# Performance work log

Hardware: AMD Instinct MI355X
Metric: run time of the kernel (lower is better)

Reference implementation:

```python
import jax, jax.numpy as jnp
import numpy as np

B, C, H, W = 8, 64, 64, 64
CI = 32  # inter_channels = in_channels // 2
EPS = 1e-5


def conv1x1(x, w, b=None):
    # x: (b,c,h,w), w: (o,c) -> (b,o,h,w)
    y = jnp.einsum('bchw,oc->bohw', x, w)
    if b is not None:
        y = y + b[None, :, None, None]
    return y


def maxpool2x2(x):
    b, c, h, w = x.shape
    return x.reshape(b, c, h // 2, 2, w // 2, 2).max(axis=(3, 5))


def setup_inputs() -> dict:
    key = jax.random.key(0)
    ks = jax.random.split(key, 12)
    s = 0.05
    return {
        'x': jax.random.normal(ks[0], (B, C, H, W), jnp.float32),
        'theta_w': jax.random.normal(ks[1], (CI, C), jnp.float32) * s,
        'theta_b': jax.random.normal(ks[2], (CI,), jnp.float32) * s,
        'phi_w': jax.random.normal(ks[3], (CI, C), jnp.float32) * s,
        'phi_b': jax.random.normal(ks[4], (CI,), jnp.float32) * s,
        'psi_w': jax.random.normal(ks[5], (CI, C), jnp.float32) * s,
        'psi_b': jax.random.normal(ks[6], (CI,), jnp.float32) * s,
        'cp_w': jax.random.normal(ks[7], (2 * CI,), jnp.float32) * s,  # concat_project 1x1, no bias
        'W_w': jax.random.normal(ks[8], (C, CI + 1), jnp.float32) * s,
        'W_b': jax.random.normal(ks[9], (C,), jnp.float32) * s,
        'bn_gamma': jax.random.normal(ks[10], (C,), jnp.float32) * s + 1.0,
        'bn_beta': jax.random.normal(ks[11], (C,), jnp.float32) * s,
    }


def reference(x, theta_w, theta_b, phi_w, phi_b, psi_w, psi_b, cp_w, W_w, W_b, bn_gamma, bn_beta):
    b = x.shape[0]
    # psi / phi branches get 2x2 maxpool (sub_sample=True default)
    psi_x = maxpool2x2(conv1x1(x, psi_w, psi_b)).reshape(b, CI, -1)      # (b,ci,M)
    psi_x = psi_x.transpose(0, 2, 1)                                     # (b,M,ci)
    theta_x = conv1x1(x, theta_w, theta_b).reshape(b, CI, -1)            # (b,ci,N)
    phi_x = maxpool2x2(conv1x1(x, phi_w, phi_b)).reshape(b, CI, -1)      # (b,ci,M)
    # concat_project(cat[theta_i, phi_j]) + ReLU == relu(w1.theta_i + w2.phi_j)
    w1, w2 = cp_w[:CI], cp_w[CI:]
    a = jnp.einsum('bcn,c->bn', theta_x, w1)                             # (b,N)
    bb = jnp.einsum('bcm,c->bm', phi_x, w2)                              # (b,M)
    f = jax.nn.relu(a[:, :, None] + bb[:, None, :])                      # (b,N,M)
    M = f.shape[-1]
    f_div_C = f / float(M)
    y = jnp.matmul(f_div_C, psi_x)                                       # (b,N,ci)
    y = y.transpose(0, 2, 1).reshape(b, CI, H, W)
    # r_structure_type='zero' -> zero structure channel
    structure_feat = jnp.zeros((b, 1, H, W), y.dtype)
    y = jnp.concatenate([y, structure_feat], axis=1)                     # (b,ci+1,H,W)
    wy = conv1x1(y, W_w, W_b)                                            # (b,C,H,W)
    # BatchNorm2d, training-mode batch stats, biased variance
    mu = wy.mean(axis=(0, 2, 3), keepdims=True)
    var = wy.var(axis=(0, 2, 3), keepdims=True)
    wy = (wy - mu) * jax.lax.rsqrt(var + EPS)
    wy = wy * bn_gamma[None, :, None, None] + bn_beta[None, :, None, None]
    return wy + x
```

## Files before the change

kernel.cpp:

```cpp
#include <hip/hip_runtime.h>

#define OFF_A    0
#define OFF_BB   32768
#define OFF_SBB  40960
#define OFF_PERM 49152
#define OFF_U    57344
#define OFF_T1   581632
#define OFF_T2   1106432
#define OFF_KK   1631232
#define OFF_M    1664000

__global__ __launch_bounds__(256) void kA(
    const float* __restrict__ x, const float* __restrict__ theta_w,
    const float* __restrict__ theta_b, const float* __restrict__ phi_w,
    const float* __restrict__ phi_b, const float* __restrict__ psi_w,
    const float* __restrict__ psi_b, const float* __restrict__ cp_w,
    const float* __restrict__ Ww, float* ws)
{
    __shared__ float sm[4160];
    __shared__ float spsi[8*33];
    __shared__ float sWw[64*33];
    int tid = threadIdx.x;
    int bid = blockIdx.x;
    if (bid < 1024) {
        for (int e = tid; e < 2048; e += 256) {
            int i = e >> 6, c = e & 63;
            sm[i*65 + c]        = phi_w[e];
            sm[2080 + i*65 + c] = psi_w[e];
        }
        for (int e = tid; e < 2048; e += 256)
            sWw[(e >> 5)*33 + (e & 31)] = Ww[(e >> 5)*33 + (e & 31)];
        __syncthreads();
        int t = (bid << 8) + tid;
        int i = t & 31;
        int m = (t >> 5) & 1023;
        int b = t >> 15;
        int ph = m >> 5, pw = m & 31;
        const float* xb = x + b*262144 + ph*128 + pw*2;
        const float* rp = sm + i*65;
        const float* rs = sm + 2080 + i*65;
        float p0=0,p1=0,p2=0,p3=0,s0=0,s1=0,s2=0,s3=0;
        #pragma unroll 8
        for (int c = 0; c < 64; ++c) {
            float2 xa = *(const float2*)(xb + c*4096);
            float2 xc = *(const float2*)(xb + c*4096 + 64);
            float wp = rp[c], wv = rs[c];
            p0 += xa.x*wp; p1 += xa.y*wp; p2 += xc.x*wp; p3 += xc.y*wp;
            s0 += xa.x*wv; s1 += xa.y*wv; s2 += xc.x*wv; s3 += xc.y*wv;
        }
        float pv = fmaxf(fmaxf(p0,p1), fmaxf(p2,p3)) + phi_b[i];
        float sv = fmaxf(fmaxf(s0,s1), fmaxf(s2,s3)) + psi_b[i];
        spsi[(tid >> 5)*33 + i] = sv;
        float v = pv * cp_w[32 + i];
        v += __shfl_xor(v, 16, 32);
        v += __shfl_xor(v,  8, 32);
        v += __shfl_xor(v,  4, 32);
        v += __shfl_xor(v,  2, 32);
        v += __shfl_xor(v,  1, 32);
        if (i == 0) ws[OFF_BB + (b<<10) + m] = v;
        __syncthreads();
        int m0 = (bid & 127) << 3;
        #pragma unroll
        for (int rep = 0; rep < 2; ++rep) {
            int idx = tid + (rep << 8);
            int ml = idx >> 6, o = idx & 63;
            const float* pr = &spsi[ml*33];
            const float* wr = &sWw[o*33];
            float u = 0;
            #pragma unroll
            for (int i2 = 0; i2 < 32; ++i2) u += pr[i2]*wr[i2];
            ws[OFF_U + (((b<<10) + m0 + ml) << 6) + o] = u;
        }
    } else {
        if (bid == 1024 && tid < 128) ws[OFF_M + tid] = 0.0f;
        if (tid < 64) {
            float s = 0;
            for (int i = 0; i < 32; ++i) s += cp_w[i]*theta_w[i*64 + tid];
            sm[tid] = s;
        } else if (tid == 64) {
            float s = 0;
            for (int i = 0; i < 32; ++i) s += cp_w[i]*theta_b[i];
            sm[64] = s;
        }
        __syncthreads();
        int t = ((bid - 1024) << 8) + tid;
        int n = t & 4095, b = t >> 12;
        const float* xb = x + b*262144 + n;
        float acc = sm[64];
        #pragma unroll 8
        for (int c = 0; c < 64; ++c) acc += xb[c*4096]*sm[c];
        ws[OFF_A + t] = acc;
    }
}

__global__ __launch_bounds__(256) void kRank(float* ws)
{
    __shared__ float sb[1024];
    int tid = threadIdx.x;
    int b = blockIdx.x >> 5, chunk = blockIdx.x & 31;
    const float* bb = ws + OFF_BB + (b<<10);
    for (int e = tid; e < 1024; e += 256) sb[e] = bb[e];
    __syncthreads();
    int ml = tid >> 3, jl = tid & 7;
    int m = (chunk<<5) + ml;
    float v = sb[m];
    int cnt = 0;
    for (int s = 0; s < 128; ++s) {
        int j = jl + (s<<3);
        float u = sb[j];
        cnt += (u > v || (u == v && j < m)) ? 1 : 0;
    }
    cnt += __shfl_xor(cnt, 1, 8);
    cnt += __shfl_xor(cnt, 2, 8);
    cnt += __shfl_xor(cnt, 4, 8);
    if (jl == 0) {
        ws[OFF_SBB + (b<<10) + cnt] = v;
        ((int*)ws)[OFF_PERM + (b<<10) + cnt] = m;
    }
}

__global__ __launch_bounds__(1024) void kPS(float* ws)
{
    __shared__ float ssort[1024];
    __shared__ int   sperm[1024];
    __shared__ float sc1[1024];
    __shared__ float sc2[1024];
    __shared__ float hcnt[1025], hsa[1025], hsa2[1025];
    int tid = threadIdx.x;
    int b = blockIdx.x >> 1, oh = blockIdx.x & 1;
    int obase = oh << 5;
    ssort[tid] = ws[OFF_SBB + (b<<10) + tid];
    sperm[tid] = ((const int*)ws)[OFF_PERM + (b<<10) + tid];
    for (int e = tid; e < 1025; e += 1024) { hcnt[e]=0; hsa[e]=0; hsa2[e]=0; }
    __syncthreads();
    const float* ag = ws + OFF_A + (b<<12);
    int* kk = (int*)ws + OFF_KK + (b<<12);
    for (int q = 0; q < 4; ++q) {
        int n = (q<<10) + tid;
        float av = ag[n];
        float tt = -av;
        int lo = 0, hi = 1024;
        #pragma unroll
        for (int s = 0; s < 10; ++s) {
            int mid = (lo+hi)>>1;
            if (ssort[mid] > tt) lo = mid+1; else hi = mid;
        }
        if (oh == 0) kk[n] = lo;
        atomicAdd(&hcnt[lo], 1.0f);
        atomicAdd(&hsa[lo], av);
        atomicAdd(&hsa2[lo], av*av);
    }
    __syncthreads();
    int o = tid & 31, ch = tid >> 5;
    const float* Ub = ws + OFF_U + (b<<16);
    float s1 = 0, s2 = 0;
    for (int jl = 0; jl < 32; ++jl) {
        int jj = (ch<<5) + jl;
        float p = Ub[(sperm[jj]<<6) + obase + o];
        s1 += p; s2 += ssort[jj]*p;
    }
    sc1[(ch<<5)+o] = s1; sc2[(ch<<5)+o] = s2;
    __syncthreads();
    if (tid < 32) {
        float run = 0;
        for (int c = 0; c < 32; ++c) { float t = sc1[(c<<5)+tid]; sc1[(c<<5)+tid] = run; run += t; }
    } else if (tid < 64) {
        int o2 = tid - 32;
        float run = 0;
        for (int c = 0; c < 32; ++c) { float t = sc2[(c<<5)+o2]; sc2[(c<<5)+o2] = run; run += t; }
    }
    __syncthreads();
    float run1 = sc1[(ch<<5)+o], run2 = sc2[(ch<<5)+o];
    float* T1 = ws + OFF_T1 + b*65600;
    float* T2 = ws + OFF_T2 + b*65600;
    if (tid < 32) { T1[obase + tid] = 0.0f; T2[obase + tid] = 0.0f; }
    const float inv = 1.0f/1024.0f;
    float m1 = 0, m2 = 0;
    for (int jl = 0; jl < 32; ++jl) {
        int jj = (ch<<5) + jl;
        float p = Ub[(sperm[jj]<<6) + obase + o];
        run1 += p; run2 += ssort[jj]*p;
        float t1 = run1*inv, t2 = run2*inv;
        int k = jj + 1;
        T1[(k<<6) + obase + o] = t1;
        T2[(k<<6) + obase + o] = t2;
        float c = hcnt[k], sa = hsa[k], sa2 = hsa2[k];
        m1 += sa*t1 + c*t2;
        m2 += sa2*t1*t1 + 2.0f*sa*t1*t2 + c*t2*t2;
    }
    __syncthreads();
    sc1[(ch<<5)+o] = m1; sc2[(ch<<5)+o] = m2;
    __syncthreads();
    if (tid < 32) {
        float s = 0;
        for (int c = 0; c < 32; ++c) s += sc1[(c<<5)+tid];
        atomicAdd(&ws[OFF_M + obase + tid], s);
    } else if (tid < 64) {
        int o2 = tid - 32;
        float s = 0;
        for (int c = 0; c < 32; ++c) s += sc2[(c<<5)+o2];
        atomicAdd(&ws[OFF_M + 64 + obase + o2], s);
    }
}

__global__ __launch_bounds__(256) void kFinal(
    const float* __restrict__ x, const float* __restrict__ Wb,
    const float* __restrict__ gamma, const float* __restrict__ beta,
    const float* __restrict__ ws, float* __restrict__ out)
{
    __shared__ float tile[64*65];
    __shared__ float sa[64];
    __shared__ int   sk[64];
    __shared__ float sA[64];
    __shared__ float sD[64];
    int tid = threadIdx.x;
    int b = blockIdx.x >> 6;
    int n0 = (blockIdx.x & 63) << 6;
    if (tid < 64) {
        sa[tid] = ws[OFF_A + (b<<12) + n0 + tid];
        sk[tid] = ((const int*)ws)[OFF_KK + (b<<12) + n0 + tid];
        const float Ninv = 1.0f/32768.0f;
        float m1 = ws[OFF_M + tid] * Ninv;
        float m2 = ws[OFF_M + 64 + tid] * Ninv;
        float wb = Wb[tid];
        float mu  = m1 + wb;
        float E2  = m2 + 2.0f*wb*m1 + wb*wb;
        float var = E2 - mu*mu;
        float A = gamma[tid] * rsqrtf(var + 1e-5f);
        sA[tid] = A;
        sD[tid] = beta[tid] + A*(wb - mu);
    }
    __syncthreads();
    const float* T1 = ws + OFF_T1 + b*65600;
    const float* T2 = ws + OFF_T2 + b*65600;
    {
        int o = tid & 63, ng = tid >> 6;
        float Ao = sA[o], Do = sD[o];
        for (int j = 0; j < 16; ++j) {
            int n = (ng << 4) + j;
            int k = sk[n];
            float a = sa[n];
            float t1 = T1[(k<<6) + o];
            float t2 = T2[(k<<6) + o];
            tile[o*65 + n] = Ao*(a*t1 + t2) + Do;
        }
    }
    __syncthreads();
    {
        int n = tid & 63, og = tid >> 6;
        for (int j = 0; j < 16; ++j) {
            int o = (og << 4) + j;
            int idx = ((b<<6) + o)*4096 + n0 + n;
            out[idx] = tile[o*65 + n] + x[idx];
        }
    }
}

extern "C" void kernel_launch(void* const* d_in, const int* in_sizes, int n_in,
                              void* d_out, int out_size, void* d_ws, size_t ws_size,
                              hipStream_t stream)
{
    const float* x       = (const float*)d_in[0];
    const float* theta_w = (const float*)d_in[1];
    const float* theta_b = (const float*)d_in[2];
    const float* phi_w   = (const float*)d_in[3];
    const float* phi_b   = (const float*)d_in[4];
    const float* psi_w   = (const float*)d_in[5];
    const float* psi_b   = (const float*)d_in[6];
    const float* cp_w    = (const float*)d_in[7];
    const float* Ww      = (const float*)d_in[8];
    const float* Wb      = (const float*)d_in[9];
    const float* gamma   = (const float*)d_in[10];
    const float* beta    = (const float*)d_in[11];
    float* ws  = (float*)d_ws;
    float* out = (float*)d_out;

    kA<<<1152, 256, 0, stream>>>(x, theta_w, theta_b, phi_w, phi_b,
                                 psi_w, psi_b, cp_w, Ww, ws);
    kRank<<<256, 256, 0, stream>>>(ws);
    kPS<<<16, 1024, 0, stream>>>(ws);
    kFinal<<<512, 256, 0, stream>>>(x, Wb, gamma, beta, ws, out);
}
```

Before: 143.0 us.

## Move threshold histogram into rank kernel and widen prefix-scan kernel across blocks

Computes the per-query insertion index and histograms by brute-force counting in kRank, accumulating them with global atomics, so kPS no longer does a binary search and shared histogram. kPS now runs 64 blocks of 8 output channels each instead of 16 blocks of 32. Its prefix scan uses wave shuffles plus a small cross-wave pass rather than serial shared-memory scans. Psi values are held in registers so U is read once. This raises parallelism in the serial-bottleneck kernel, at the cost of extra global atomics and a larger zero-init in kA.

```diff
diff --git a/kernel.cpp b/kernel.cpp
--- a/kernel.cpp
+++ b/kernel.cpp
@@ -9,6 +9,9 @@
 #define OFF_T2   1106432
 #define OFF_KK   1631232
 #define OFF_M    1664000
+#define OFF_HC   1664128
+#define OFF_HS   1672328
+#define OFF_HS2  1680528
 
 __global__ __launch_bounds__(256) void kA(
     const float* __restrict__ x, const float* __restrict__ theta_w,
@@ -72,7 +75,9 @@
             ws[OFF_U + (((b<<10) + m0 + ml) << 6) + o] = u;
         }
     } else {
-        if (bid == 1024 && tid < 128) ws[OFF_M + tid] = 0.0f;
+        if (bid == 1024) {
+            for (int e = tid; e < 24728; e += 256) ws[OFF_M + e] = 0.0f;
+        }
         if (tid < 64) {
             float s = 0;
             for (int i = 0; i < 32; ++i) s += cp_w[i]*theta_w[i*64 + tid];
@@ -101,21 +106,43 @@
     const float* bb = ws + OFF_BB + (b<<10);
     for (int e = tid; e < 1024; e += 256) sb[e] = bb[e];
     __syncthreads();
-    int ml = tid >> 3, jl = tid & 7;
-    int m = (chunk<<5) + ml;
-    float v = sb[m];
-    int cnt = 0;
-    for (int s = 0; s < 128; ++s) {
-        int j = jl + (s<<3);
-        float u = sb[j];
-        cnt += (u > v || (u == v && j < m)) ? 1 : 0;
-    }
-    cnt += __shfl_xor(cnt, 1, 8);
-    cnt += __shfl_xor(cnt, 2, 8);
-    cnt += __shfl_xor(cnt, 4, 8);
-    if (jl == 0) {
-        ws[OFF_SBB + (b<<10) + cnt] = v;
-        ((int*)ws)[OFF_PERM + (b<<10) + cnt] = m;
+    {
+        int ml = tid >> 3, jl = tid & 7;
+        int m = (chunk<<5) + ml;
+        float v = sb[m];
+        int cnt = 0;
+        for (int s = 0; s < 128; ++s) {
+            int j = jl + (s<<3);
+            float u = sb[j];
+            cnt += (u > v || (u == v && j < m)) ? 1 : 0;
+        }
+        cnt += __shfl_xor(cnt, 1, 8);
+        cnt += __shfl_xor(cnt, 2, 8);
+        cnt += __shfl_xor(cnt, 4, 8);
+        if (jl == 0) {
+            ws[OFF_SBB + (b<<10) + cnt] = v;
+            ((int*)ws)[OFF_PERM + (b<<10) + cnt] = m;
+        }
+    }
+    {
+        int l = tid >> 1, jl = tid & 1;
+        int n = (chunk<<7) + l;
+        float av = ws[OFF_A + (b<<12) + n];
+        float tt = -av;
+        const float2* sb2 = (const float2*)sb;
+        int cnt = 0;
+        for (int s = 0; s < 256; ++s) {
+            float2 u = sb2[jl + (s<<1)];
+            cnt += (u.x > tt) ? 1 : 0;
+            cnt += (u.y > tt) ? 1 : 0;
+        }
+        cnt += __shfl_xor(cnt, 1, 64);
+        if (jl == 0) {
+            ((int*)ws)[OFF_KK + (b<<12) + n] = cnt;
+            atomicAdd(&ws[OFF_HC + b*1025 + cnt], 1.0f);
+            atomicAdd(&ws[OFF_HS + b*1025 + cnt], av);
+            atomicAdd(&ws[OFF_HS2 + b*1025 + cnt], av*av);
+        }
     }
 }
 
@@ -123,83 +150,77 @@
 {
     __shared__ float ssort[1024];
     __shared__ int   sperm[1024];
-    __shared__ float sc1[1024];
-    __shared__ float sc2[1024];
-    __shared__ float hcnt[1025], hsa[1025], hsa2[1025];
+    __shared__ float shc[1025], shs[1025], shs2[1025];
+    __shared__ float swp1[128], swp2[128];
     int tid = threadIdx.x;
-    int b = blockIdx.x >> 1, oh = blockIdx.x & 1;
-    int obase = oh << 5;
+    int b = blockIdx.x >> 3, og = blockIdx.x & 7;
+    int obase = og << 3;
     ssort[tid] = ws[OFF_SBB + (b<<10) + tid];
     sperm[tid] = ((const int*)ws)[OFF_PERM + (b<<10) + tid];
-    for (int e = tid; e < 1025; e += 1024) { hcnt[e]=0; hsa[e]=0; hsa2[e]=0; }
-    __syncthreads();
-    const float* ag = ws + OFF_A + (b<<12);
-    int* kk = (int*)ws + OFF_KK + (b<<12);
-    for (int q = 0; q < 4; ++q) {
-        int n = (q<<10) + tid;
-        float av = ag[n];
-        float tt = -av;
-        int lo = 0, hi = 1024;
-        #pragma unroll
-        for (int s = 0; s < 10; ++s) {
-            int mid = (lo+hi)>>1;
-            if (ssort[mid] > tt) lo = mid+1; else hi = mid;
-        }
-        if (oh == 0) kk[n] = lo;
-        atomicAdd(&hcnt[lo], 1.0f);
-        atomicAdd(&hsa[lo], av);
-        atomicAdd(&hsa2[lo], av*av);
-    }
-    __syncthreads();
-    int o = tid & 31, ch = tid >> 5;
-    const float* Ub = ws + OFF_U + (b<<16);
+    shc[tid]  = ws[OFF_HC  + b*1025 + tid];
+    shs[tid]  = ws[OFF_HS  + b*1025 + tid];
+    shs2[tid] = ws[OFF_HS2 + b*1025 + tid];
+    if (tid == 0) {
+        shc[1024]  = ws[OFF_HC  + b*1025 + 1024];
+        shs[1024]  = ws[OFF_HS  + b*1025 + 1024];
+        shs2[1024] = ws[OFF_HS2 + b*1025 + 1024];
+    }
+    __syncthreads();
+    int ch = tid >> 3, o = tid & 7;
+    int wv = tid >> 6, chl = (tid & 63) >> 3;
+    const float* Ub = ws + OFF_U + (b<<16) + obase + o;
+    float p[8], sp[8];
     float s1 = 0, s2 = 0;
-    for (int jl = 0; jl < 32; ++jl) {
-        int jj = (ch<<5) + jl;
-        float p = Ub[(sperm[jj]<<6) + obase + o];
-        s1 += p; s2 += ssort[jj]*p;
-    }
-    sc1[(ch<<5)+o] = s1; sc2[(ch<<5)+o] = s2;
-    __syncthreads();
-    if (tid < 32) {
-        float run = 0;
-        for (int c = 0; c < 32; ++c) { float t = sc1[(c<<5)+tid]; sc1[(c<<5)+tid] = run; run += t; }
-    } else if (tid < 64) {
-        int o2 = tid - 32;
-        float run = 0;
-        for (int c = 0; c < 32; ++c) { float t = sc2[(c<<5)+o2]; sc2[(c<<5)+o2] = run; run += t; }
-    }
-    __syncthreads();
-    float run1 = sc1[(ch<<5)+o], run2 = sc2[(ch<<5)+o];
-    float* T1 = ws + OFF_T1 + b*65600;
-    float* T2 = ws + OFF_T2 + b*65600;
-    if (tid < 32) { T1[obase + tid] = 0.0f; T2[obase + tid] = 0.0f; }
+    #pragma unroll
+    for (int jl = 0; jl < 8; ++jl) {
+        int jj = (ch<<3) + jl;
+        float v = Ub[sperm[jj]<<6];
+        p[jl] = v;
+        sp[jl] = ssort[jj]*v;
+        s1 += v; s2 += sp[jl];
+    }
+    float own1 = s1, own2 = s2;
+    #pragma unroll
+    for (int d = 1; d < 8; d <<= 1) {
+        float u1 = __shfl_up(s1, d<<3, 64);
+        float u2 = __shfl_up(s2, d<<3, 64);
+        if (chl >= d) { s1 += u1; s2 += u2; }
+    }
+    if (chl == 7) { swp1[(wv<<3)+o] = s1; swp2[(wv<<3)+o] = s2; }
+    __syncthreads();
+    float off1 = 0, off2 = 0;
+    for (int w = 0; w < 16; ++w) {
+        if (w < wv) { off1 += swp1[(w<<3)+o]; off2 += swp2[(w<<3)+o]; }
+    }
+    float run1 = off1 + s1 - own1;
+    float run2 = off2 + s2 - own2;
+    float* T1 = ws + OFF_T1 + b*65600 + obase + o;
+    float* T2 = ws + OFF_T2 + b*65600 + obase + o;
+    if (ch == 0) { T1[0] = 0.0f; T2[0] = 0.0f; }
     const float inv = 1.0f/1024.0f;
     float m1 = 0, m2 = 0;
-    for (int jl = 0; jl < 32; ++jl) {
-        int jj = (ch<<5) + jl;
-        float p = Ub[(sperm[jj]<<6) + obase + o];
-        run1 += p; run2 += ssort[jj]*p;
+    #pragma unroll
+    for (int jl = 0; jl < 8; ++jl) {
+        int k = (ch<<3) + jl + 1;
+        run1 += p[jl]; run2 += sp[jl];
         float t1 = run1*inv, t2 = run2*inv;
-        int k = jj + 1;
-        T1[(k<<6) + obase + o] = t1;
-        T2[(k<<6) + obase + o] = t2;
-        float c = hcnt[k], sa = hsa[k], sa2 = hsa2[k];
+        T1[k<<6] = t1;
+        T2[k<<6] = t2;
+        float c = shc[k], sa = shs[k], sa2 = shs2[k];
         m1 += sa*t1 + c*t2;
-        m2 += sa2*t1*t1 + 2.0f*sa*t1*t2 + c*t2*t2;
-    }
-    __syncthreads();
-    sc1[(ch<<5)+o] = m1; sc2[(ch<<5)+o] = m2;
-    __syncthreads();
-    if (tid < 32) {
-        float s = 0;
-        for (int c = 0; c < 32; ++c) s += sc1[(c<<5)+tid];
-        atomicAdd(&ws[OFF_M + obase + tid], s);
-    } else if (tid < 64) {
-        int o2 = tid - 32;
-        float s = 0;
-        for (int c = 0; c < 32; ++c) s += sc2[(c<<5)+o2];
-        atomicAdd(&ws[OFF_M + 64 + obase + o2], s);
+        m2 += (sa2*t1 + 2.0f*sa*t2)*t1 + c*t2*t2;
+    }
+    m1 += __shfl_xor(m1,  8, 64); m2 += __shfl_xor(m2,  8, 64);
+    m1 += __shfl_xor(m1, 16, 64); m2 += __shfl_xor(m2, 16, 64);
+    m1 += __shfl_xor(m1, 32, 64); m2 += __shfl_xor(m2, 32, 64);
+    __syncthreads();
+    if (chl == 0) { swp1[(wv<<3)+o] = m1; swp2[(wv<<3)+o] = m2; }
+    __syncthreads();
+    if (tid < 8) {
+        float a1 = 0, a2 = 0;
+        for (int w = 0; w < 16; ++w) { a1 += swp1[(w<<3)+tid]; a2 += swp2[(w<<3)+tid]; }
+        atomicAdd(&ws[OFF_M + obase + tid], a1);
+        atomicAdd(&ws[OFF_M + 64 + obase + tid], a2);
     }
 }
 
@@ -278,6 +299,6 @@
     kA<<<1152, 256, 0, stream>>>(x, theta_w, theta_b, phi_w, phi_b,
                                  psi_w, psi_b, cp_w, Ww, ws);
     kRank<<<256, 256, 0, stream>>>(ws);
-    kPS<<<16, 1024, 0, stream>>>(ws);
+    kPS<<<64, 1024, 0, stream>>>(ws);
     kFinal<<<512, 256, 0, stream>>>(x, Wb, gamma, beta, ws, out);
 }
```

Measured after the change: 132.9 us. 1.08x faster.
